# Kernel tuning notes

Hardware: AMD Instinct MI355X
Metric: run time of the kernel (lower is better)

## Reference

```python
import jax, jax.numpy as jnp
import numpy as np

N, E = 50000, 800000
HID, EDIM, HEADS = 256, 64, 8
C = HID // HEADS  # per-head channels = 32
NEG_SLOPE = 0.2
LN_EPS = 1e-5


def setup_inputs() -> dict:
    key = jax.random.key(0)
    ks = jax.random.split(key, 12)
    s = 1.0 / np.sqrt(HID)
    se = 1.0 / np.sqrt(EDIM)
    return {
        "x": jax.random.normal(ks[0], (N, HID), jnp.float32),
        "edge_index": jax.random.randint(ks[1], (2, E), 0, N, jnp.int32),
        "edge_attr": jax.random.normal(ks[2], (E, EDIM), jnp.float32),
        "W": jax.random.uniform(ks[3], (HID, HEADS * C), jnp.float32, -s, s),
        "W_e": jax.random.uniform(ks[4], (EDIM, HEADS * C), jnp.float32, -se, se),
        "att_src": jax.random.normal(ks[5], (HEADS, C), jnp.float32) * 0.1,
        "att_dst": jax.random.normal(ks[6], (HEADS, C), jnp.float32) * 0.1,
        "att_edge": jax.random.normal(ks[7], (HEADS, C), jnp.float32) * 0.1,
        "bias": jnp.zeros((HEADS * C,), jnp.float32),
        "gamma": jnp.ones((HID,), jnp.float32),
        "beta": jnp.zeros((HID,), jnp.float32),
    }


def _gat_block(x, edge_index, edge_attr, W, W_e, att_src, att_dst, att_edge, bias, gamma, beta):
    n = x.shape[0]
    src, dst = edge_index[0], edge_index[1]
    # node projection (shared for src/dst, as in PyG GATConv non-bipartite)
    xp = (x @ W).reshape(n, HEADS, C)                       # [N,H,C]
    a_src = jnp.einsum("nhc,hc->nh", xp, att_src)          # [N,H]
    a_dst = jnp.einsum("nhc,hc->nh", xp, att_dst)          # [N,H]
    ep = (edge_attr @ W_e).reshape(-1, HEADS, C)            # [E,H,C]
    a_edge = jnp.einsum("ehc,hc->eh", ep, att_edge)        # [E,H]
    # per-edge attention logit + LeakyReLU
    alpha = a_src[src] + a_dst[dst] + a_edge                # [E,H]
    alpha = jax.nn.leaky_relu(alpha, NEG_SLOPE)
    # segment softmax over incoming edges of each dst node
    m = jax.ops.segment_max(alpha, dst, num_segments=n)     # [N,H]
    m = jnp.where(jnp.isfinite(m), m, 0.0)
    ea = jnp.exp(alpha - m[dst])
    den = jax.ops.segment_sum(ea, dst, num_segments=n)      # [N,H]
    attn = ea / (den[dst] + 1e-16)                          # [E,H]
    # weighted message + scatter-add
    msg = xp[src] * attn[:, :, None]                        # [E,H,C]
    out = jax.ops.segment_sum(msg, dst, num_segments=n)     # [N,H,C]
    h = out.reshape(n, HEADS * C) + bias
    # residual + LayerNorm (dropout in eval mode -> identity)
    y = x + h
    mu = jnp.mean(y, axis=-1, keepdims=True)
    var = jnp.var(y, axis=-1, keepdims=True)
    return (y - mu) * jax.lax.rsqrt(var + LN_EPS) * gamma + beta


def reference(x, edge_index, edge_attr, W, W_e, att_src, att_dst, att_edge, bias, gamma, beta):
    return _gat_block(x, edge_index, edge_attr, W, W_e, att_src, att_dst, att_edge, bias, gamma, beta)
```

## Files before the change

### kernel.cpp

```cpp
#include <hip/hip_runtime.h>
#include <cstdint>

#define NEG_SLOPE 0.2f
#define LN_EPS 1e-5f

typedef __bf16 bf16x8 __attribute__((ext_vector_type(8)));
typedef float f32x4 __attribute__((ext_vector_type(4)));

__device__ __forceinline__ float b2f(unsigned int u) {
    union { unsigned int i; float f; } x; x.i = u << 16; return x.f;
}
__device__ __forceinline__ unsigned short f2b(float f) {
    union { float f; unsigned int i; } x; x.f = f;
    unsigned int r = x.i + 0x7fffu + ((x.i >> 16) & 1u);
    return (unsigned short)(r >> 16);
}

__global__ void k0a_prep(const float* __restrict__ W,
                         const float* __restrict__ We,
                         const float* __restrict__ att_src,
                         const float* __restrict__ att_dst,
                         const float* __restrict__ att_edge,
                         float* __restrict__ u_src, float* __restrict__ u_dst,
                         float* __restrict__ vW) {
    int t = threadIdx.x;
    const float* wr = W + t * 256;
    for (int h = 0; h < 8; h++) {
        float s1 = 0.f, s2 = 0.f;
        for (int c = 0; c < 32; c++) {
            float w = wr[h * 32 + c];
            s1 += w * att_src[h * 32 + c];
            s2 += w * att_dst[h * 32 + c];
        }
        u_src[t * 8 + h] = s1; u_dst[t * 8 + h] = s2;
    }
    if (t < 64) {
        const float* er = We + t * 256;
        for (int h = 0; h < 8; h++) {
            float s = 0.f;
            for (int c = 0; c < 32; c++) s += er[h * 32 + c] * att_edge[h * 32 + c];
            vW[t * 8 + h] = s;
        }
    }
}

__global__ void k0b_transpose(const float* __restrict__ W,
                              unsigned short* __restrict__ Wt) {
    int n = blockIdx.x;
    int k = threadIdx.x;
    Wt[n * 256 + k] = f2b(W[k * 256 + n]);
}

__global__ __launch_bounds__(256) void k1_xp(const float* __restrict__ x,
                                             const unsigned short* __restrict__ Wt,
                                             unsigned short* __restrict__ xp, int N) {
    int m0 = blockIdx.x * 16;
    int lane = threadIdx.x & 63, wave = threadIdx.x >> 6;
    int quad = lane >> 4, l16 = lane & 15;
    int mrow = m0 + l16; if (mrow > N - 1) mrow = N - 1;
    const float* ap = x + mrow * 256 + quad * 8;
    const unsigned short* bp0 = Wt + (wave * 64 + l16) * 256 + quad * 8;
    const unsigned short* bp1 = bp0 + 16 * 256;
    const unsigned short* bp2 = bp0 + 32 * 256;
    const unsigned short* bp3 = bp0 + 48 * 256;
    f32x4 ac0 = {0,0,0,0}, ac1 = {0,0,0,0}, ac2 = {0,0,0,0}, ac3 = {0,0,0,0};
#pragma unroll
    for (int kk = 0; kk < 8; kk++) {
        float4 fa0 = *(const float4*)(ap + kk * 32);
        float4 fa1 = *(const float4*)(ap + kk * 32 + 4);
        union { unsigned short u[8]; bf16x8 v; } A;
        A.u[0] = f2b(fa0.x); A.u[1] = f2b(fa0.y); A.u[2] = f2b(fa0.z); A.u[3] = f2b(fa0.w);
        A.u[4] = f2b(fa1.x); A.u[5] = f2b(fa1.y); A.u[6] = f2b(fa1.z); A.u[7] = f2b(fa1.w);
        bf16x8 b0 = *(const bf16x8*)(bp0 + kk * 32);
        bf16x8 b1 = *(const bf16x8*)(bp1 + kk * 32);
        bf16x8 b2 = *(const bf16x8*)(bp2 + kk * 32);
        bf16x8 b3 = *(const bf16x8*)(bp3 + kk * 32);
        ac0 = __builtin_amdgcn_mfma_f32_16x16x32_bf16(A.v, b0, ac0, 0, 0, 0);
        ac1 = __builtin_amdgcn_mfma_f32_16x16x32_bf16(A.v, b1, ac1, 0, 0, 0);
        ac2 = __builtin_amdgcn_mfma_f32_16x16x32_bf16(A.v, b2, ac2, 0, 0, 0);
        ac3 = __builtin_amdgcn_mfma_f32_16x16x32_bf16(A.v, b3, ac3, 0, 0, 0);
    }
    int nb = wave * 64;
#pragma unroll
    for (int r = 0; r < 4; r++) {
        int m = m0 + quad * 4 + r;
        if (m < N) {
            unsigned short* op = xp + m * 256 + nb + l16;
            op[0]  = f2b(ac0[r]); op[16] = f2b(ac1[r]);
            op[32] = f2b(ac2[r]); op[48] = f2b(ac3[r]);
        }
    }
}

__global__ __launch_bounds__(256) void k1b_ad(const float* __restrict__ x,
                                              const float* __restrict__ u_src,
                                              const float* __restrict__ u_dst,
                                              float* __restrict__ a_src,
                                              float* __restrict__ a_dst, int N) {
    int n = blockIdx.x * 256 + threadIdx.x;
    if (n >= N) return;
    const float4* xr = (const float4*)(x + n * 256);
    float as[8] = {0,0,0,0,0,0,0,0}, ad[8] = {0,0,0,0,0,0,0,0};
    for (int kk = 0; kk < 64; kk++) {
        float4 u = xr[kk];
        float f[4] = {u.x, u.y, u.z, u.w};
#pragma unroll
        for (int j = 0; j < 4; j++) {
            int k = kk * 4 + j;
#pragma unroll
            for (int h = 0; h < 8; h++) {
                as[h] += f[j] * u_src[k * 8 + h];
                ad[h] += f[j] * u_dst[k * 8 + h];
            }
        }
    }
    float4* po = (float4*)(a_src + n * 8);
    po[0] = make_float4(as[0], as[1], as[2], as[3]);
    po[1] = make_float4(as[4], as[5], as[6], as[7]);
    float4* pd = (float4*)(a_dst + n * 8);
    pd[0] = make_float4(ad[0], ad[1], ad[2], ad[3]);
    pd[1] = make_float4(ad[4], ad[5], ad[6], ad[7]);
}

__global__ __launch_bounds__(256) void k2_edge(const int* __restrict__ ei,
                                               const float* __restrict__ eattr,
                                               const float* __restrict__ vW,
                                               const float* __restrict__ a_src,
                                               const float* __restrict__ a_dst,
                                               unsigned short* __restrict__ ea,
                                               int* __restrict__ deg, int E) {
    int e = blockIdx.x * 256 + threadIdx.x;
    if (e >= E) return;
    int s = ei[e], d = ei[E + e];
    float acc[8] = {0,0,0,0,0,0,0,0};
    const float4* ar = (const float4*)(eattr + (size_t)e * 64);
    for (int kk = 0; kk < 16; kk++) {
        float4 u = ar[kk];
        float f[4] = {u.x, u.y, u.z, u.w};
#pragma unroll
        for (int j = 0; j < 4; j++) {
            int k = kk * 4 + j;
#pragma unroll
            for (int h = 0; h < 8; h++) acc[h] += f[j] * vW[k * 8 + h];
        }
    }
    const float4* asp = (const float4*)(a_src + s * 8);
    const float4* adp = (const float4*)(a_dst + d * 8);
    float4 as0 = asp[0], as1 = asp[1], ad0 = adp[0], ad1 = adp[1];
    float asv[8] = {as0.x, as0.y, as0.z, as0.w, as1.x, as1.y, as1.z, as1.w};
    float adv[8] = {ad0.x, ad0.y, ad0.z, ad0.w, ad1.x, ad1.y, ad1.z, ad1.w};
    unsigned short pk[8];
#pragma unroll
    for (int h = 0; h < 8; h++) {
        float al = asv[h] + adv[h] + acc[h];
        al = (al > 0.f) ? al : NEG_SLOPE * al;
        pk[h] = f2b(__expf(al));
    }
    uint4 st;
    st.x = (unsigned)pk[0] | ((unsigned)pk[1] << 16);
    st.y = (unsigned)pk[2] | ((unsigned)pk[3] << 16);
    st.z = (unsigned)pk[4] | ((unsigned)pk[5] << 16);
    st.w = (unsigned)pk[6] | ((unsigned)pk[7] << 16);
    ((uint4*)ea)[e] = st;
    atomicAdd(deg + d, 1);
}

__global__ __launch_bounds__(1024) void k3a_scan(const int* __restrict__ deg,
                                                 int* __restrict__ rowptr,
                                                 int* __restrict__ bsum, int N) {
    __shared__ int s[1024];
    int t = threadIdx.x, i = blockIdx.x * 1024 + t;
    int v = (i < N) ? deg[i] : 0;
    s[t] = v; __syncthreads();
    for (int off = 1; off < 1024; off <<= 1) {
        int add = (t >= off) ? s[t - off] : 0;
        __syncthreads();
        s[t] += add;
        __syncthreads();
    }
    if (i < N) rowptr[i] = s[t] - v;
    if (t == 1023) bsum[blockIdx.x] = s[1023];
}
__global__ void k3b_scan(const int* __restrict__ bsum, int* __restrict__ boff, int nb) {
    if (threadIdx.x == 0) {
        int run = 0;
        for (int i = 0; i < nb; i++) { boff[i] = run; run += bsum[i]; }
    }
}
__global__ __launch_bounds__(1024) void k3c_add(int* __restrict__ rowptr,
                                                int* __restrict__ cursor,
                                                const int* __restrict__ boff, int N, int E) {
    int i = blockIdx.x * 1024 + threadIdx.x;
    if (i < N) {
        int r = rowptr[i] + boff[blockIdx.x];
        rowptr[i] = r; cursor[i] = r;
    }
    if (i == 0) rowptr[N] = E;
}
__global__ __launch_bounds__(256) void k3d_scatter(const int* __restrict__ ei,
                                                   int* __restrict__ cursor,
                                                   int* __restrict__ perm, int E) {
    int e = blockIdx.x * 256 + threadIdx.x;
    if (e >= E) return;
    int d = ei[E + e];
    int p = atomicAdd(cursor + d, 1);
    perm[p] = e;
}

__global__ __launch_bounds__(64) void k4_agg(const float* __restrict__ xin,
                                             const unsigned short* __restrict__ xp,
                                             const unsigned short* __restrict__ ea,
                                             const int* __restrict__ rowptr,
                                             const int* __restrict__ perm,
                                             const int* __restrict__ ei,
                                             const float* __restrict__ bias,
                                             const float* __restrict__ gamma,
                                             const float* __restrict__ beta,
                                             float* __restrict__ out, int N) {
    __shared__ int ssrc[64];
    __shared__ float sattn[64 * 9];
    int n = blockIdx.x, l = threadIdx.x;
    int start = rowptr[n], end = rowptr[n + 1];

    float dl[8] = {0,0,0,0,0,0,0,0};
    for (int base = start; base < end; base += 64) {
        if (base + l < end) {
            int e = perm[base + l];
            uint4 u = ((const uint4*)ea)[e];
            dl[0] += b2f(u.x & 0xffffu); dl[1] += b2f(u.x >> 16);
            dl[2] += b2f(u.y & 0xffffu); dl[3] += b2f(u.y >> 16);
            dl[4] += b2f(u.z & 0xffffu); dl[5] += b2f(u.z >> 16);
            dl[6] += b2f(u.w & 0xffffu); dl[7] += b2f(u.w >> 16);
        }
    }
#pragma unroll
    for (int off = 32; off > 0; off >>= 1) {
#pragma unroll
        for (int j = 0; j < 8; j++) dl[j] += __shfl_xor(dl[j], off, 64);
    }
    float sinv[8];
#pragma unroll
    for (int j = 0; j < 8; j++) sinv[j] = 1.0f / (dl[j] + 1e-16f);

    float a0 = 0.f, a1 = 0.f, a2 = 0.f, a3 = 0.f;
    int hh = l >> 3;
    for (int base = start; base < end; base += 64) {
        int cnt = end - base; if (cnt > 64) cnt = 64;
        if (l < cnt) {
            int e = perm[base + l];
            ssrc[l] = ei[e];
            uint4 u = ((const uint4*)ea)[e];
            float* sp = sattn + l * 9;
            sp[0] = b2f(u.x & 0xffffu) * sinv[0]; sp[1] = b2f(u.x >> 16) * sinv[1];
            sp[2] = b2f(u.y & 0xffffu) * sinv[2]; sp[3] = b2f(u.y >> 16) * sinv[3];
            sp[4] = b2f(u.z & 0xffffu) * sinv[4]; sp[5] = b2f(u.z >> 16) * sinv[5];
            sp[6] = b2f(u.w & 0xffffu) * sinv[6]; sp[7] = b2f(u.w >> 16) * sinv[7];
        }
        __syncthreads();
        for (int i = 0; i < cnt; i++) {
            int s = ssrc[i];
            uint2 u = *(const uint2*)(xp + s * 256 + l * 4);
            float w = sattn[i * 9 + hh];
            a0 += b2f(u.x & 0xffffu) * w; a1 += b2f(u.x >> 16) * w;
            a2 += b2f(u.y & 0xffffu) * w; a3 += b2f(u.y >> 16) * w;
        }
        __syncthreads();
    }
    float4 xv = *(const float4*)(xin + n * 256 + l * 4);
    float4 bv = *(const float4*)(bias + l * 4);
    float y0 = xv.x + a0 + bv.x;
    float y1 = xv.y + a1 + bv.y;
    float y2 = xv.z + a2 + bv.z;
    float y3 = xv.w + a3 + bv.w;
    float s1 = y0 + y1 + y2 + y3;
    float s2 = y0 * y0 + y1 * y1 + y2 * y2 + y3 * y3;
#pragma unroll
    for (int o = 32; o > 0; o >>= 1) {
        s1 += __shfl_down(s1, o, 64);
        s2 += __shfl_down(s2, o, 64);
    }
    s1 = __shfl(s1, 0, 64); s2 = __shfl(s2, 0, 64);
    float mu = s1 * (1.f / 256.f);
    float var = s2 * (1.f / 256.f) - mu * mu;
    float rs = rsqrtf(var + LN_EPS);
    float4 gv  = *(const float4*)(gamma + l * 4);
    float4 btv = *(const float4*)(beta + l * 4);
    float4 ov;
    ov.x = (y0 - mu) * rs * gv.x + btv.x;
    ov.y = (y1 - mu) * rs * gv.y + btv.y;
    ov.z = (y2 - mu) * rs * gv.z + btv.z;
    ov.w = (y3 - mu) * rs * gv.w + btv.w;
    *(float4*)(out + n * 256 + l * 4) = ov;
}

extern "C" void kernel_launch(void* const* d_in, const int* in_sizes, int n_in,
                              void* d_out, int out_size, void* d_ws, size_t ws_size,
                              hipStream_t stream) {
    const float* x     = (const float*)d_in[0];
    const int*   ei    = (const int*)d_in[1];
    const float* eattr = (const float*)d_in[2];
    const float* W     = (const float*)d_in[3];
    const float* We    = (const float*)d_in[4];
    const float* atts  = (const float*)d_in[5];
    const float* attd  = (const float*)d_in[6];
    const float* atte  = (const float*)d_in[7];
    const float* bias  = (const float*)d_in[8];
    const float* gamma = (const float*)d_in[9];
    const float* beta  = (const float*)d_in[10];
    float* out = (float*)d_out;
    int N = in_sizes[0] / 256;
    int E = in_sizes[1] / 2;

    char* p = (char*)d_ws;
    auto carve = [&](size_t bytes) -> void* {
        void* r = (void*)p; p += (bytes + 255) & ~(size_t)255; return r;
    };
    unsigned short* xp = (unsigned short*)carve((size_t)N * 256 * 2);
    unsigned short* ea = (unsigned short*)carve((size_t)E * 8 * 2);
    float* a_src       = (float*)carve((size_t)N * 8 * 4);
    float* a_dst       = (float*)carve((size_t)N * 8 * 4);
    int*   deg         = (int*)carve((size_t)N * 4);
    int*   rowptr      = (int*)carve((size_t)(N + 1) * 4);
    int*   cursor      = (int*)carve((size_t)N * 4);
    int*   perm        = (int*)carve((size_t)E * 4);
    int*   bsum        = (int*)carve(1024);
    int*   boff        = (int*)carve(1024);
    float* u_src       = (float*)carve(2048 * 4);
    float* u_dst       = (float*)carve(2048 * 4);
    float* vW          = (float*)carve(512 * 4);
    unsigned short* Wt = (unsigned short*)carve(65536 * 2);

    hipMemsetAsync(deg, 0, (size_t)N * 4, stream);

    hipLaunchKernelGGL(k0a_prep, dim3(1), dim3(256), 0, stream,
                       W, We, atts, attd, atte, u_src, u_dst, vW);
    hipLaunchKernelGGL(k0b_transpose, dim3(256), dim3(256), 0, stream, W, Wt);
    hipLaunchKernelGGL(k1_xp, dim3((N + 15) / 16), dim3(256), 0, stream, x, Wt, xp, N);
    hipLaunchKernelGGL(k1b_ad, dim3((N + 255) / 256), dim3(256), 0, stream,
                       x, u_src, u_dst, a_src, a_dst, N);
    hipLaunchKernelGGL(k2_edge, dim3((E + 255) / 256), dim3(256), 0, stream,
                       ei, eattr, vW, a_src, a_dst, ea, deg, E);
    int nb = (N + 1023) / 1024;
    hipLaunchKernelGGL(k3a_scan, dim3(nb), dim3(1024), 0, stream, deg, rowptr, bsum, N);
    hipLaunchKernelGGL(k3b_scan, dim3(1), dim3(64), 0, stream, bsum, boff, nb);
    hipLaunchKernelGGL(k3c_add, dim3(nb), dim3(1024), 0, stream, rowptr, cursor, boff, N, E);
    hipLaunchKernelGGL(k3d_scatter, dim3((E + 255) / 256), dim3(256), 0, stream,
                       ei, cursor, perm, E);
    hipLaunchKernelGGL(k4_agg, dim3(N), dim3(64), 0, stream,
                       x, xp, ea, rowptr, perm, ei, bias, gamma, beta, out, N);
}
```

Before: 668.1 us.

## Fuse attention-score projection into xp GEMM and split edge logits across lanes

The separate a_src/a_dst kernel is folded into the MFMA projection kernel. Each wave computes partial dot products for its quarter of K from the x values it already loads, and the partials are combined through shuffles and shared memory. This removes a second full read of x. W is pre-laid-out in MFMA fragment order so B loads become contiguous per lane. The edge kernel now uses four threads per edge with vW staged in shared memory, giving coalesced edge_attr reads and lower per-thread register and serial work, at the cost of extra shuffles and a block barrier.

```diff
diff --git a/kernel.cpp b/kernel.cpp
--- a/kernel.cpp
+++ b/kernel.cpp
@@ -44,82 +44,106 @@
     }
 }
 
-__global__ void k0b_transpose(const float* __restrict__ W,
-                              unsigned short* __restrict__ Wt) {
-    int n = blockIdx.x;
-    int k = threadIdx.x;
-    Wt[n * 256 + k] = f2b(W[k * 256 + n]);
+__global__ void k0b_wfrag(const float* __restrict__ W,
+                          unsigned short* __restrict__ Wf) {
+    int T = blockIdx.x * 256 + threadIdx.x;
+    int j    = T & 7;
+    int lane = (T >> 3) & 63;
+    int kk   = (T >> 9) & 7;
+    int i    = (T >> 12) & 3;
+    int w    = T >> 14;
+    int n = w * 64 + i * 16 + (lane & 15);
+    int k = kk * 32 + (lane >> 4) * 8 + j;
+    Wf[T] = f2b(W[k * 256 + n]);
 }
 
 __global__ __launch_bounds__(256) void k1_xp(const float* __restrict__ x,
-                                             const unsigned short* __restrict__ Wt,
-                                             unsigned short* __restrict__ xp, int N) {
+                                             const unsigned short* __restrict__ Wf,
+                                             const float* __restrict__ u_src,
+                                             const float* __restrict__ u_dst,
+                                             unsigned short* __restrict__ xp,
+                                             float* __restrict__ a_src,
+                                             float* __restrict__ a_dst, int N) {
+    __shared__ float red[2][4][16][8];
     int m0 = blockIdx.x * 16;
     int lane = threadIdx.x & 63, wave = threadIdx.x >> 6;
     int quad = lane >> 4, l16 = lane & 15;
     int mrow = m0 + l16; if (mrow > N - 1) mrow = N - 1;
-    const float* ap = x + mrow * 256 + quad * 8;
-    const unsigned short* bp0 = Wt + (wave * 64 + l16) * 256 + quad * 8;
-    const unsigned short* bp1 = bp0 + 16 * 256;
-    const unsigned short* bp2 = bp0 + 32 * 256;
-    const unsigned short* bp3 = bp0 + 48 * 256;
+    const float* ap = x + (size_t)mrow * 256 + quad * 8;
+    const unsigned short* wfw = Wf + (size_t)wave * 16384;
     f32x4 ac0 = {0,0,0,0}, ac1 = {0,0,0,0}, ac2 = {0,0,0,0}, ac3 = {0,0,0,0};
+    float pas[8] = {0,0,0,0,0,0,0,0}, pad_[8] = {0,0,0,0,0,0,0,0};
 #pragma unroll
     for (int kk = 0; kk < 8; kk++) {
         float4 fa0 = *(const float4*)(ap + kk * 32);
         float4 fa1 = *(const float4*)(ap + kk * 32 + 4);
+        if ((kk >> 1) == wave) {
+            float f[8] = {fa0.x, fa0.y, fa0.z, fa0.w, fa1.x, fa1.y, fa1.z, fa1.w};
+#pragma unroll
+            for (int j = 0; j < 8; j++) {
+                int k = kk * 32 + quad * 8 + j;
+                const float4* up = (const float4*)(u_src + k * 8);
+                float4 s0 = up[0], s1 = up[1];
+                const float4* vp = (const float4*)(u_dst + k * 8);
+                float4 d0 = vp[0], d1 = vp[1];
+                pas[0] += f[j] * s0.x; pas[1] += f[j] * s0.y;
+                pas[2] += f[j] * s0.z; pas[3] += f[j] * s0.w;
+                pas[4] += f[j] * s1.x; pas[5] += f[j] * s1.y;
+                pas[6] += f[j] * s1.z; pas[7] += f[j] * s1.w;
+                pad_[0] += f[j] * d0.x; pad_[1] += f[j] * d0.y;
+                pad_[2] += f[j] * d0.z; pad_[3] += f[j] * d0.w;
+                pad_[4] += f[j] * d1.x; pad_[5] += f[j] * d1.y;
+                pad_[6] += f[j] * d1.z; pad_[7] += f[j] * d1.w;
+            }
+        }
         union { unsigned short u[8]; bf16x8 v; } A;
         A.u[0] = f2b(fa0.x); A.u[1] = f2b(fa0.y); A.u[2] = f2b(fa0.z); A.u[3] = f2b(fa0.w);
         A.u[4] = f2b(fa1.x); A.u[5] = f2b(fa1.y); A.u[6] = f2b(fa1.z); A.u[7] = f2b(fa1.w);
-        bf16x8 b0 = *(const bf16x8*)(bp0 + kk * 32);
-        bf16x8 b1 = *(const bf16x8*)(bp1 + kk * 32);
-        bf16x8 b2 = *(const bf16x8*)(bp2 + kk * 32);
-        bf16x8 b3 = *(const bf16x8*)(bp3 + kk * 32);
+        const unsigned short* wk = wfw + kk * 512 + lane * 8;
+        bf16x8 b0 = *(const bf16x8*)(wk);
+        bf16x8 b1 = *(const bf16x8*)(wk + 4096);
+        bf16x8 b2 = *(const bf16x8*)(wk + 8192);
+        bf16x8 b3 = *(const bf16x8*)(wk + 12288);
         ac0 = __builtin_amdgcn_mfma_f32_16x16x32_bf16(A.v, b0, ac0, 0, 0, 0);
         ac1 = __builtin_amdgcn_mfma_f32_16x16x32_bf16(A.v, b1, ac1, 0, 0, 0);
         ac2 = __builtin_amdgcn_mfma_f32_16x16x32_bf16(A.v, b2, ac2, 0, 0, 0);
         ac3 = __builtin_amdgcn_mfma_f32_16x16x32_bf16(A.v, b3, ac3, 0, 0, 0);
     }
+#pragma unroll
+    for (int h = 0; h < 8; h++) {
+        pas[h] += __shfl_xor(pas[h], 16, 64);
+        pas[h] += __shfl_xor(pas[h], 32, 64);
+        pad_[h] += __shfl_xor(pad_[h], 16, 64);
+        pad_[h] += __shfl_xor(pad_[h], 32, 64);
+    }
+    if (quad == 0) {
+#pragma unroll
+        for (int h = 0; h < 8; h++) {
+            red[0][wave][l16][h] = pas[h];
+            red[1][wave][l16][h] = pad_[h];
+        }
+    }
     int nb = wave * 64;
 #pragma unroll
     for (int r = 0; r < 4; r++) {
         int m = m0 + quad * 4 + r;
         if (m < N) {
-            unsigned short* op = xp + m * 256 + nb + l16;
+            unsigned short* op = xp + (size_t)m * 256 + nb + l16;
             op[0]  = f2b(ac0[r]); op[16] = f2b(ac1[r]);
             op[32] = f2b(ac2[r]); op[48] = f2b(ac3[r]);
         }
     }
-}
-
-__global__ __launch_bounds__(256) void k1b_ad(const float* __restrict__ x,
-                                              const float* __restrict__ u_src,
-                                              const float* __restrict__ u_dst,
-                                              float* __restrict__ a_src,
-                                              float* __restrict__ a_dst, int N) {
-    int n = blockIdx.x * 256 + threadIdx.x;
-    if (n >= N) return;
-    const float4* xr = (const float4*)(x + n * 256);
-    float as[8] = {0,0,0,0,0,0,0,0}, ad[8] = {0,0,0,0,0,0,0,0};
-    for (int kk = 0; kk < 64; kk++) {
-        float4 u = xr[kk];
-        float f[4] = {u.x, u.y, u.z, u.w};
-#pragma unroll
-        for (int j = 0; j < 4; j++) {
-            int k = kk * 4 + j;
-#pragma unroll
-            for (int h = 0; h < 8; h++) {
-                as[h] += f[j] * u_src[k * 8 + h];
-                ad[h] += f[j] * u_dst[k * 8 + h];
-            }
-        }
-    }
-    float4* po = (float4*)(a_src + n * 8);
-    po[0] = make_float4(as[0], as[1], as[2], as[3]);
-    po[1] = make_float4(as[4], as[5], as[6], as[7]);
-    float4* pd = (float4*)(a_dst + n * 8);
-    pd[0] = make_float4(ad[0], ad[1], ad[2], ad[3]);
-    pd[1] = make_float4(ad[4], ad[5], ad[6], ad[7]);
+    __syncthreads();
+    {
+        int t = threadIdx.x;
+        int arr = t >> 7, r = (t >> 3) & 15, h = t & 7;
+        int m = m0 + r;
+        if (m < N) {
+            float sum = red[arr][0][r][h] + red[arr][1][r][h]
+                      + red[arr][2][r][h] + red[arr][3][r][h];
+            (arr ? a_dst : a_src)[m * 8 + h] = sum;
+        }
+    }
 }
 
 __global__ __launch_bounds__(256) void k2_edge(const int* __restrict__ ei,
@@ -129,40 +153,50 @@
                                                const float* __restrict__ a_dst,
                                                unsigned short* __restrict__ ea,
                                                int* __restrict__ deg, int E) {
-    int e = blockIdx.x * 256 + threadIdx.x;
+    __shared__ float sv[2048];
+    int t = threadIdx.x;
+    if (t < 128) {
+        const float4* g = (const float4*)vW;
+        float4* s4 = (float4*)sv;
+        int k = t >> 1, half = t & 1;
+        int kl = ((k & 15) << 2) | (k >> 4);
+        s4[kl * 2 + half] = g[t];
+    }
+    __syncthreads();
+    int e = blockIdx.x * 64 + (t >> 2), kp = t & 3;
     if (e >= E) return;
+    const float4* ar = (const float4*)(eattr + (size_t)e * 64 + kp * 16);
+    float acc[8] = {0,0,0,0,0,0,0,0};
+#pragma unroll
+    for (int q = 0; q < 4; q++) {
+        float4 u = ar[q];
+        float f[4] = {u.x, u.y, u.z, u.w};
+#pragma unroll
+        for (int j = 0; j < 4; j++) {
+            int kl = ((q * 4 + j) << 2) | kp;
+            const float4* vp = (const float4*)(sv + kl * 8);
+            float4 v0 = vp[0], v1 = vp[1];
+            acc[0] += f[j] * v0.x; acc[1] += f[j] * v0.y;
+            acc[2] += f[j] * v0.z; acc[3] += f[j] * v0.w;
+            acc[4] += f[j] * v1.x; acc[5] += f[j] * v1.y;
+            acc[6] += f[j] * v1.z; acc[7] += f[j] * v1.w;
+        }
+    }
+#pragma unroll
+    for (int h = 0; h < 8; h++) {
+        acc[h] += __shfl_xor(acc[h], 1, 64);
+        acc[h] += __shfl_xor(acc[h], 2, 64);
+    }
     int s = ei[e], d = ei[E + e];
-    float acc[8] = {0,0,0,0,0,0,0,0};
-    const float4* ar = (const float4*)(eattr + (size_t)e * 64);
-    for (int kk = 0; kk < 16; kk++) {
-        float4 u = ar[kk];
-        float f[4] = {u.x, u.y, u.z, u.w};
-#pragma unroll
-        for (int j = 0; j < 4; j++) {
-            int k = kk * 4 + j;
-#pragma unroll
-            for (int h = 0; h < 8; h++) acc[h] += f[j] * vW[k * 8 + h];
-        }
-    }
-    const float4* asp = (const float4*)(a_src + s * 8);
-    const float4* adp = (const float4*)(a_dst + d * 8);
-    float4 as0 = asp[0], as1 = asp[1], ad0 = adp[0], ad1 = adp[1];
-    float asv[8] = {as0.x, as0.y, as0.z, as0.w, as1.x, as1.y, as1.z, as1.w};
-    float adv[8] = {ad0.x, ad0.y, ad0.z, ad0.w, ad1.x, ad1.y, ad1.z, ad1.w};
-    unsigned short pk[8];
-#pragma unroll
-    for (int h = 0; h < 8; h++) {
-        float al = asv[h] + adv[h] + acc[h];
-        al = (al > 0.f) ? al : NEG_SLOPE * al;
-        pk[h] = f2b(__expf(al));
-    }
-    uint4 st;
-    st.x = (unsigned)pk[0] | ((unsigned)pk[1] << 16);
-    st.y = (unsigned)pk[2] | ((unsigned)pk[3] << 16);
-    st.z = (unsigned)pk[4] | ((unsigned)pk[5] << 16);
-    st.w = (unsigned)pk[6] | ((unsigned)pk[7] << 16);
-    ((uint4*)ea)[e] = st;
-    atomicAdd(deg + d, 1);
+    float2 asv = *(const float2*)(a_src + s * 8 + kp * 2);
+    float2 adv = *(const float2*)(a_dst + d * 8 + kp * 2);
+    float l0 = asv.x + adv.x + acc[kp * 2];
+    float l1 = asv.y + adv.y + acc[kp * 2 + 1];
+    l0 = (l0 > 0.f) ? l0 : NEG_SLOPE * l0;
+    l1 = (l1 > 0.f) ? l1 : NEG_SLOPE * l1;
+    unsigned int pk = (unsigned)f2b(__expf(l0)) | ((unsigned)f2b(__expf(l1)) << 16);
+    ((unsigned int*)ea)[(size_t)e * 4 + kp] = pk;
+    if (kp == 0) atomicAdd(deg + d, 1);
 }
 
 __global__ __launch_bounds__(1024) void k3a_scan(const int* __restrict__ deg,
@@ -259,14 +293,14 @@
         __syncthreads();
         for (int i = 0; i < cnt; i++) {
             int s = ssrc[i];
-            uint2 u = *(const uint2*)(xp + s * 256 + l * 4);
+            uint2 u = *(const uint2*)(xp + (size_t)s * 256 + l * 4);
             float w = sattn[i * 9 + hh];
             a0 += b2f(u.x & 0xffffu) * w; a1 += b2f(u.x >> 16) * w;
             a2 += b2f(u.y & 0xffffu) * w; a3 += b2f(u.y >> 16) * w;
         }
         __syncthreads();
     }
-    float4 xv = *(const float4*)(xin + n * 256 + l * 4);
+    float4 xv = *(const float4*)(xin + (size_t)n * 256 + l * 4);
     float4 bv = *(const float4*)(bias + l * 4);
     float y0 = xv.x + a0 + bv.x;
     float y1 = xv.y + a1 + bv.y;
@@ -290,7 +324,7 @@
     ov.y = (y1 - mu) * rs * gv.y + btv.y;
     ov.z = (y2 - mu) * rs * gv.z + btv.z;
     ov.w = (y3 - mu) * rs * gv.w + btv.w;
-    *(float4*)(out + n * 256 + l * 4) = ov;
+    *(float4*)(out + (size_t)n * 256 + l * 4) = ov;
 }
 
 extern "C" void kernel_launch(void* const* d_in, const int* in_sizes, int n_in,
@@ -328,17 +362,16 @@
     float* u_src       = (float*)carve(2048 * 4);
     float* u_dst       = (float*)carve(2048 * 4);
     float* vW          = (float*)carve(512 * 4);
-    unsigned short* Wt = (unsigned short*)carve(65536 * 2);
+    unsigned short* Wf = (unsigned short*)carve(65536 * 2);
 
     hipMemsetAsync(deg, 0, (size_t)N * 4, stream);
 
     hipLaunchKernelGGL(k0a_prep, dim3(1), dim3(256), 0, stream,
                        W, We, atts, attd, atte, u_src, u_dst, vW);
-    hipLaunchKernelGGL(k0b_transpose, dim3(256), dim3(256), 0, stream, W, Wt);
-    hipLaunchKernelGGL(k1_xp, dim3((N + 15) / 16), dim3(256), 0, stream, x, Wt, xp, N);
-    hipLaunchKernelGGL(k1b_ad, dim3((N + 255) / 256), dim3(256), 0, stream,
-                       x, u_src, u_dst, a_src, a_dst, N);
-    hipLaunchKernelGGL(k2_edge, dim3((E + 255) / 256), dim3(256), 0, stream,
+    hipLaunchKernelGGL(k0b_wfrag, dim3(256), dim3(256), 0, stream, W, Wf);
+    hipLaunchKernelGGL(k1_xp, dim3((N + 15) / 16), dim3(256), 0, stream,
+                       x, Wf, u_src, u_dst, xp, a_src, a_dst, N);
+    hipLaunchKernelGGL(k2_edge, dim3((E + 63) / 64), dim3(256), 0, stream,
                        ei, eattr, vW, a_src, a_dst, ea, deg, E);
     int nb = (N + 1023) / 1024;
     hipLaunchKernelGGL(k3a_scan, dim3(nb), dim3(1024), 0, stream, deg, rowptr, bsum, N);
```

After: 610.8 us. -8.6%, faster.
